# Optimization experiments

Hardware: AMD Instinct MI355X
Metric: run time of the kernel (lower is better)

Reference implementation:

```python
import jax, jax.numpy as jnp
import numpy as np

B, D, E, H, T = 16384, 32, 8, 64, 10  # batch, state_dim, n_experts, hidden, time points
TEMP = 1.0  # gating temperature


def setup_inputs() -> dict:
    key = jax.random.key(0)
    ks = jax.random.split(key, 12)
    w = lambda k, shape, fan_in: (jax.random.normal(k, shape, jnp.float32) / np.sqrt(fan_in)).astype(jnp.float32)
    return {
        "x0": jax.random.normal(ks[0], (B, D), jnp.float32),
        "t_span": jnp.linspace(0.0, 1.0, T).astype(jnp.float32),
        # per-expert time-conditioned MLP: (x, t) -> H -> H -> D
        "W1": w(ks[1], (E, D + 1, H), D + 1), "b1": jnp.zeros((E, H), jnp.float32),
        "W2": w(ks[2], (E, H, H), H),          "b2": jnp.zeros((E, H), jnp.float32),
        "W3": w(ks[3], (E, H, D), H),          "b3": jnp.zeros((E, D), jnp.float32),
        # gating MLP on concat(x, dx_init): 2D -> H -> E
        "Gw1": w(ks[4], (2 * D, H), 2 * D), "Gb1": jnp.zeros((H,), jnp.float32),
        "Gw2": w(ks[5], (H, E), H),         "Gb2": jnp.zeros((E,), jnp.float32),
    }


def _dyn(t, x, W1, b1, W2, b2, W3, b3, Gw1, Gb1, Gw2, Gb2):
    # AME-ODE training-path dynamics: uniform-weighted init, gate, weighted sum
    inp = jnp.concatenate([x, jnp.ones((x.shape[0], 1), x.dtype) * t], axis=-1)  # [B, D+1]
    h = jnp.tanh(jnp.einsum('bi,eih->beh', inp, W1) + b1)
    h = jnp.tanh(jnp.einsum('beh,ehg->beg', h, W2) + b2)
    f = jnp.einsum('beg,egd->bed', h, W3) + b3          # all-expert dynamics [B, E, D]
    dx_init = f.mean(axis=1)                             # uniform weights 1/E
    g = jnp.tanh(jnp.concatenate([x, dx_init], -1) @ Gw1 + Gb1)
    wgt = jax.nn.softmax((g @ Gw2 + Gb2) / TEMP, axis=-1)  # [B, E]
    return jnp.einsum('be,bed->bd', wgt, f)


def reference(x0, t_span, W1, b1, W2, b2, W3, b3, Gw1, Gb1, Gw2, Gb2):
    params = (W1, b1, W2, b2, W3, b3, Gw1, Gb1, Gw2, Gb2)

    def step(x, ts):
        t0, t1 = ts[0], ts[1]
        dt = t1 - t0
        k1 = _dyn(t0, x, *params)
        k2 = _dyn(t0 + 0.5 * dt, x + 0.5 * dt * k1, *params)
        k3 = _dyn(t0 + 0.5 * dt, x + 0.5 * dt * k2, *params)
        k4 = _dyn(t1, x + dt * k3, *params)
        xn = x + (dt / 6.0) * (k1 + 2.0 * k2 + 2.0 * k3 + k4)
        return xn, xn

    pairs = jnp.stack([t_span[:-1], t_span[1:]], axis=1)  # [T-1, 2]
    _, traj = jax.lax.scan(step, x0, pairs)               # [T-1, B, D]
    traj = jnp.concatenate([x0[None], traj], axis=0)       # [T, B, D]
    return jnp.transpose(traj, (1, 0, 2))                  # [B, T, D]
```

## Files before the change

kernel.cpp:

```cpp
#include <hip/hip_runtime.h>
#include <hip/hip_bf16.h>

typedef unsigned int u32;
typedef unsigned short u16;
typedef __attribute__((ext_vector_type(8))) short short8;
typedef __attribute__((ext_vector_type(4))) float f32x4;
typedef __attribute__((ext_vector_type(4))) u32 u32x4;

#define DD 32
#define EE 8
#define HH 64
#define TT 10
#define BATCH 16384
#define EPB 32

__device__ __forceinline__ float fast_tanh(float x) {
  float e = __expf(2.f * x);
  return 1.f - 2.f * __builtin_amdgcn_rcpf(e + 1.f);
}
__device__ __forceinline__ u16 f2b_rn(float v) {
  return (u16)((__float_as_uint(v) + 0x8000u) >> 16);
}
__device__ __forceinline__ u32 pack2_rn(float a, float b) {
  return ((__float_as_uint(a) + 0x8000u) >> 16) |
         ((__float_as_uint(b) + 0x8000u) & 0xffff0000u);
}
__device__ __forceinline__ float unp_lo(u32 p) { return __uint_as_float(p << 16); }
__device__ __forceinline__ float unp_hi(u32 p) { return __uint_as_float(p & 0xffff0000u); }
__device__ __forceinline__ short8 lds_frag(const u32* p) {
  u32x4 w = *(const u32x4*)p;
  return __builtin_bit_cast(short8, w);
}

__global__ __launch_bounds__(512) void ame_ode_kernel(
    const float* __restrict__ x0, const float* __restrict__ tspan,
    const float* __restrict__ W1, const float* __restrict__ b1,
    const float* __restrict__ W2, const float* __restrict__ b2,
    const float* __restrict__ W3, const float* __restrict__ b3,
    const float* __restrict__ Gw1, const float* __restrict__ Gb1,
    const float* __restrict__ Gw2, const float* __restrict__ Gb2,
    float* __restrict__ out)
{
  __shared__ __align__(16) u32 xdb[EPB][36];
  __shared__ __align__(16) u32 fs[EPB][130];
  __shared__ __align__(16) float lg[EPB][9];
  __shared__ __align__(16) u32 hsbuf[EE * 16 * 36];
  __shared__ __align__(16) u16 gw1t[HH][72];
  __shared__ __align__(16) u16 gw2t[16][72];

  const int tid  = threadIdx.x;
  const int lane = tid & 63;
  const int l15  = lane & 15;
  const int quad = lane >> 4;
  const int e    = __builtin_amdgcn_readfirstlane(tid >> 6);
  const int elem = lane & 31;
  const int hf   = lane >> 5;
  const int cc   = 2 * e + hf;
  const int d0   = 2 * cc;
  const int bglob = blockIdx.x * EPB;

  const float* W1f = W1 + e * (DD + 1) * HH;
  const float* b1f = b1 + e * HH;
  const float* W2f = W2 + e * HH * HH;
  const float* b2f = b2 + e * HH;
  const float* W3f = W3 + e * HH * DD;
  const float* b3f = b3 + e * DD;

  short8 bw1[4], bw2[2][4], bw3[2][2];
  #pragma unroll
  for (int nt = 0; nt < 4; nt++)
    #pragma unroll
    for (int j = 0; j < 8; j++)
      bw1[nt][j] = (short)f2b_rn(W1f[(quad * 8 + j) * HH + nt * 16 + l15]);
  #pragma unroll
  for (int ks = 0; ks < 2; ks++)
    #pragma unroll
    for (int nt = 0; nt < 4; nt++)
      #pragma unroll
      for (int j = 0; j < 8; j++)
        bw2[ks][nt][j] = (short)f2b_rn(W2f[(ks * 32 + quad * 8 + j) * HH + nt * 16 + l15]);
  #pragma unroll
  for (int ks = 0; ks < 2; ks++)
    #pragma unroll
    for (int dt2 = 0; dt2 < 2; dt2++)
      #pragma unroll
      for (int j = 0; j < 8; j++)
        bw3[ks][dt2][j] = (short)f2b_rn(W3f[(ks * 32 + quad * 8 + j) * DD + dt2 * 16 + l15]);

  u32 c1p[4], c2p[2], c3p;
  #pragma unroll
  for (int nt = 0; nt < 4; nt++)
    c1p[nt] = pack2_rn(b1f[nt * 16 + l15], W1f[DD * HH + nt * 16 + l15]);
  #pragma unroll
  for (int p = 0; p < 2; p++)
    c2p[p] = pack2_rn(b2f[(2 * p) * 16 + l15], b2f[(2 * p + 1) * 16 + l15]);
  c3p = pack2_rn(b3f[l15], b3f[16 + l15]);
  const float gb1v = Gb1[(e >> 1) * 16 + l15];
  const float gb2v = (l15 < 8) ? Gb2[l15] : 0.f;

  for (int idx = tid; idx < HH * HH; idx += 512) {
    int h = idx >> 6, i = idx & 63;
    gw1t[h][i] = f2b_rn(Gw1[i * HH + h]);
  }
  for (int idx = tid; idx < 16 * HH; idx += 512) {
    int j = idx >> 6, h = idx & 63;
    gw2t[j][h] = (j < EE) ? f2b_rn(Gw2[h * EE + j]) : (u16)0;
  }

  float xst0, xst1, xac0, xac1;
  {
    const float2 v = *(const float2*)(x0 + (bglob + elem) * DD + d0);
    xst0 = v.x; xst1 = v.y; xac0 = v.x; xac1 = v.y;
    xdb[elem][cc] = pack2_rn(v.x, v.y);
    *(float2*)(out + ((bglob + elem) * TT) * DD + d0) = v;
  }
  __syncthreads();

  u32* const hw = hsbuf + e * 576;
  u16* const hw16 = (u16*)hw;
  u16* const fw16 = (u16*)&fs[0][0];
  const u32* const gw1t32 = (const u32*)&gw1t[0][0];
  const u32* const gw2t32 = (const u32*)&gw2t[0][0];
  const u16* const gs16 = (const u16*)hsbuf;
  u16* const gsw16 = (u16*)hsbuf;

  #pragma unroll 1
  for (int step = 0; step < TT - 1; step++) {
    const float t0 = tspan[step];
    const float t1 = tspan[step + 1];
    const float dt = t1 - t0;

    #pragma unroll 1
    for (int s = 0; s < 4; s++) {
      const float tcur = (s == 0) ? t0 : ((s == 3) ? t1 : t0 + 0.5f * dt);

      #pragma unroll
      for (int mt = 0; mt < 2; mt++) {
        const short8 a1 = lds_frag(&xdb[mt * 16 + l15][quad * 4]);
        f32x4 h1a[4];
        #pragma unroll
        for (int nt = 0; nt < 4; nt++) {
          const float iv = __builtin_fmaf(tcur, unp_hi(c1p[nt]), unp_lo(c1p[nt]));
          f32x4 c; c[0] = iv; c[1] = iv; c[2] = iv; c[3] = iv;
          h1a[nt] = __builtin_amdgcn_mfma_f32_16x16x32_bf16(a1, bw1[nt], c, 0, 0, 0);
        }
        #pragma unroll
        for (int nt = 0; nt < 4; nt++)
          #pragma unroll
          for (int r = 0; r < 4; r++)
            hw16[(quad * 4 + r) * 72 + nt * 16 + l15] = f2b_rn(fast_tanh(h1a[nt][r]));

        f32x4 h2a[4];
        #pragma unroll
        for (int nt = 0; nt < 4; nt++) {
          const float bv = (nt & 1) ? unp_hi(c2p[nt >> 1]) : unp_lo(c2p[nt >> 1]);
          f32x4 c; c[0] = bv; c[1] = bv; c[2] = bv; c[3] = bv;
          h2a[nt] = c;
        }
        #pragma unroll
        for (int ks = 0; ks < 2; ks++) {
          const short8 a2 = lds_frag(&hw[l15 * 36 + ks * 16 + quad * 4]);
          #pragma unroll
          for (int nt = 0; nt < 4; nt++)
            h2a[nt] = __builtin_amdgcn_mfma_f32_16x16x32_bf16(a2, bw2[ks][nt], h2a[nt], 0, 0, 0);
        }
        #pragma unroll
        for (int nt = 0; nt < 4; nt++)
          #pragma unroll
          for (int r = 0; r < 4; r++)
            hw16[(quad * 4 + r) * 72 + nt * 16 + l15] = f2b_rn(fast_tanh(h2a[nt][r]));

        f32x4 fa[2];
        #pragma unroll
        for (int dt2 = 0; dt2 < 2; dt2++) {
          const float bv = dt2 ? unp_hi(c3p) : unp_lo(c3p);
          f32x4 c; c[0] = bv; c[1] = bv; c[2] = bv; c[3] = bv;
          fa[dt2] = c;
        }
        #pragma unroll
        for (int ks = 0; ks < 2; ks++) {
          const short8 a3 = lds_frag(&hw[l15 * 36 + ks * 16 + quad * 4]);
          #pragma unroll
          for (int dt2 = 0; dt2 < 2; dt2++)
            fa[dt2] = __builtin_amdgcn_mfma_f32_16x16x32_bf16(a3, bw3[ks][dt2], fa[dt2], 0, 0, 0);
        }
        #pragma unroll
        for (int dt2 = 0; dt2 < 2; dt2++)
          #pragma unroll
          for (int r = 0; r < 4; r++)
            fw16[(mt * 16 + quad * 4 + r) * 260 + e * 32 + dt2 * 16 + l15] = f2b_rn(fa[dt2][r]);
      }
      __syncthreads();

      {
        float s0 = 0.f, s1 = 0.f;
        #pragma unroll
        for (int j = 0; j < EE; j++) {
          const u32 p = fs[elem][j * 16 + cc];
          s0 += unp_lo(p); s1 += unp_hi(p);
        }
        xdb[elem][16 + cc] = pack2_rn(s0 * 0.125f, s1 * 0.125f);
      }
      __syncthreads();

      {
        const int mt = e & 1, nt = e >> 1;
        f32x4 u; u[0] = gb1v; u[1] = gb1v; u[2] = gb1v; u[3] = gb1v;
        #pragma unroll
        for (int ks = 0; ks < 2; ks++) {
          const short8 ag = lds_frag(&xdb[mt * 16 + l15][ks * 16 + quad * 4]);
          const short8 bg = lds_frag(&gw1t32[(nt * 16 + l15) * 36 + ks * 16 + quad * 4]);
          u = __builtin_amdgcn_mfma_f32_16x16x32_bf16(ag, bg, u, 0, 0, 0);
        }
        #pragma unroll
        for (int r = 0; r < 4; r++)
          gsw16[(mt * 16 + quad * 4 + r) * 72 + nt * 16 + l15] = f2b_rn(fast_tanh(u[r]));
      }
      __syncthreads();

      if (e < 2) {
        const int mt = e;
        f32x4 lv; lv[0] = gb2v; lv[1] = gb2v; lv[2] = gb2v; lv[3] = gb2v;
        #pragma unroll
        for (int ks = 0; ks < 2; ks++) {
          const short8 ag = lds_frag((const u32*)&gs16[(mt * 16 + l15) * 72 + ks * 32 + quad * 8]);
          const short8 bg = lds_frag(&gw2t32[l15 * 36 + ks * 16 + quad * 4]);
          lv = __builtin_amdgcn_mfma_f32_16x16x32_bf16(ag, bg, lv, 0, 0, 0);
        }
        if (l15 < 8) {
          #pragma unroll
          for (int r = 0; r < 4; r++)
            lg[mt * 16 + quad * 4 + r][l15] = lv[r];
        }
      }
      __syncthreads();

      {
        float la[EE];
        #pragma unroll
        for (int j = 0; j < EE; j++) la[j] = lg[elem][j];
        float m = la[0];
        #pragma unroll
        for (int j = 1; j < EE; j++) m = fmaxf(m, la[j]);
        float w8[EE], ss = 0.f;
        #pragma unroll
        for (int j = 0; j < EE; j++) { w8[j] = __expf(la[j] - m); ss += w8[j]; }
        const float inv = __builtin_amdgcn_rcpf(ss);

        float k0 = 0.f, k1 = 0.f;
        #pragma unroll
        for (int j = 0; j < EE; j++) {
          const float wg = w8[j] * inv;
          const u32 p = fs[elem][j * 16 + cc];
          k0 = __builtin_fmaf(wg, unp_lo(p), k0);
          k1 = __builtin_fmaf(wg, unp_hi(p), k1);
        }

        const float wk = (s == 1 || s == 2) ? 2.f : 1.f;
        const float ak = dt * (1.f / 6.f) * wk;
        xac0 = __builtin_fmaf(ak, k0, xac0);
        xac1 = __builtin_fmaf(ak, k1, xac1);

        float xn0, xn1;
        if (s < 3) {
          const float cn = (s == 2) ? dt : 0.5f * dt;
          xn0 = __builtin_fmaf(cn, k0, xst0);
          xn1 = __builtin_fmaf(cn, k1, xst1);
        } else {
          xst0 = xac0; xst1 = xac1; xn0 = xac0; xn1 = xac1;
          float2 o; o.x = xn0; o.y = xn1;
          *(float2*)(out + ((bglob + elem) * TT + step + 1) * DD + d0) = o;
        }
        xdb[elem][cc] = pack2_rn(xn0, xn1);
      }
      __syncthreads();
    }
  }
}

extern "C" void kernel_launch(void* const* d_in, const int* in_sizes, int n_in,
                              void* d_out, int out_size, void* d_ws, size_t ws_size,
                              hipStream_t stream)
{
  const float* x0    = (const float*)d_in[0];
  const float* tspan = (const float*)d_in[1];
  const float* W1  = (const float*)d_in[2];
  const float* b1  = (const float*)d_in[3];
  const float* W2  = (const float*)d_in[4];
  const float* b2  = (const float*)d_in[5];
  const float* W3  = (const float*)d_in[6];
  const float* b3  = (const float*)d_in[7];
  const float* Gw1 = (const float*)d_in[8];
  const float* Gb1 = (const float*)d_in[9];
  const float* Gw2 = (const float*)d_in[10];
  const float* Gb2 = (const float*)d_in[11];

  ame_ode_kernel<<<BATCH / EPB, 512, 0, stream>>>(
      x0, tspan, W1, b1, W2, b2, W3, b3, Gw1, Gb1, Gw2, Gb2, (float*)d_out);
}
```

Baseline: 370.4 us.

## Double batch tile per block and keep gating weights in registers

Raises the number of batch elements per 512-thread block from 32 to 64, so each wave handles four M-tiles and all 64 lanes own one element with four state dims. The gating MLP weights move out of transposed LDS copies into per-wave register fragments, and both gating layers are spread over more waves. Biases are pre-broadcast once per stage and bf16 packing uses a single perm instruction. This amortises barriers and per-stage setup over more work, but halves the grid to 256 blocks and raises register and LDS pressure.

```diff
diff --git a/kernel.cpp b/kernel.cpp
--- a/kernel.cpp
+++ b/kernel.cpp
@@ -6,13 +6,14 @@
 typedef __attribute__((ext_vector_type(8))) short short8;
 typedef __attribute__((ext_vector_type(4))) float f32x4;
 typedef __attribute__((ext_vector_type(4))) u32 u32x4;
+typedef __attribute__((ext_vector_type(2))) u32 u32x2;
 
 #define DD 32
 #define EE 8
 #define HH 64
 #define TT 10
 #define BATCH 16384
-#define EPB 32
+#define EPB 64
 
 __device__ __forceinline__ float fast_tanh(float x) {
   float e = __expf(2.f * x);
@@ -22,8 +23,8 @@
   return (u16)((__float_as_uint(v) + 0x8000u) >> 16);
 }
 __device__ __forceinline__ u32 pack2_rn(float a, float b) {
-  return ((__float_as_uint(a) + 0x8000u) >> 16) |
-         ((__float_as_uint(b) + 0x8000u) & 0xffff0000u);
+  return __builtin_amdgcn_perm(__float_as_uint(b) + 0x8000u,
+                               __float_as_uint(a) + 0x8000u, 0x07060302u);
 }
 __device__ __forceinline__ float unp_lo(u32 p) { return __uint_as_float(p << 16); }
 __device__ __forceinline__ float unp_hi(u32 p) { return __uint_as_float(p & 0xffff0000u); }
@@ -31,6 +32,7 @@
   u32x4 w = *(const u32x4*)p;
   return __builtin_bit_cast(short8, w);
 }
+__device__ __forceinline__ f32x4 bcast4(float v) { f32x4 c; c[0]=v; c[1]=v; c[2]=v; c[3]=v; return c; }
 
 __global__ __launch_bounds__(512) void ame_ode_kernel(
     const float* __restrict__ x0, const float* __restrict__ tspan,
@@ -43,21 +45,15 @@
 {
   __shared__ __align__(16) u32 xdb[EPB][36];
   __shared__ __align__(16) u32 fs[EPB][130];
-  __shared__ __align__(16) float lg[EPB][9];
+  __shared__ __align__(16) float lg[EPB][12];
   __shared__ __align__(16) u32 hsbuf[EE * 16 * 36];
-  __shared__ __align__(16) u16 gw1t[HH][72];
-  __shared__ __align__(16) u16 gw2t[16][72];
 
   const int tid  = threadIdx.x;
   const int lane = tid & 63;
   const int l15  = lane & 15;
   const int quad = lane >> 4;
   const int e    = __builtin_amdgcn_readfirstlane(tid >> 6);
-  const int elem = lane & 31;
-  const int hf   = lane >> 5;
-  const int cc   = 2 * e + hf;
-  const int d0   = 2 * cc;
-  const int bglob = blockIdx.x * EPB;
+  const int b    = blockIdx.x * EPB + lane;
 
   const float* W1f = W1 + e * (DD + 1) * HH;
   const float* b1f = b1 + e * HH;
@@ -87,42 +83,56 @@
       for (int j = 0; j < 8; j++)
         bw3[ks][dt2][j] = (short)f2b_rn(W3f[(ks * 32 + quad * 8 + j) * DD + dt2 * 16 + l15]);
 
-  u32 c1p[4], c2p[2], c3p;
+  const int g1mt = e & 3;
+  const int g1n0 = (e >> 2) * 2;
+  short8 bg1[2][2];
+  #pragma unroll
+  for (int ni = 0; ni < 2; ni++)
+    #pragma unroll
+    for (int ks = 0; ks < 2; ks++)
+      #pragma unroll
+      for (int j = 0; j < 8; j++)
+        bg1[ni][ks][j] = (short)f2b_rn(Gw1[(ks * 32 + quad * 8 + j) * HH + (g1n0 + ni) * 16 + l15]);
+  const float gb1a = Gb1[g1n0 * 16 + l15];
+  const float gb1b = Gb1[(g1n0 + 1) * 16 + l15];
+
+  short8 bg2[2];
+  float gb2v = 0.f;
+  if (e < 4) {
+    #pragma unroll
+    for (int ks = 0; ks < 2; ks++)
+      #pragma unroll
+      for (int j = 0; j < 8; j++)
+        bg2[ks][j] = (short)((l15 < 8) ? f2b_rn(Gw2[(ks * 32 + quad * 8 + j) * EE + l15]) : 0);
+    gb2v = (l15 < 8) ? Gb2[l15] : 0.f;
+  }
+
+  u32 c1p[4];
   #pragma unroll
   for (int nt = 0; nt < 4; nt++)
     c1p[nt] = pack2_rn(b1f[nt * 16 + l15], W1f[DD * HH + nt * 16 + l15]);
-  #pragma unroll
-  for (int p = 0; p < 2; p++)
-    c2p[p] = pack2_rn(b2f[(2 * p) * 16 + l15], b2f[(2 * p + 1) * 16 + l15]);
-  c3p = pack2_rn(b3f[l15], b3f[16 + l15]);
-  const float gb1v = Gb1[(e >> 1) * 16 + l15];
-  const float gb2v = (l15 < 8) ? Gb2[l15] : 0.f;
-
-  for (int idx = tid; idx < HH * HH; idx += 512) {
-    int h = idx >> 6, i = idx & 63;
-    gw1t[h][i] = f2b_rn(Gw1[i * HH + h]);
-  }
-  for (int idx = tid; idx < 16 * HH; idx += 512) {
-    int j = idx >> 6, h = idx & 63;
-    gw2t[j][h] = (j < EE) ? f2b_rn(Gw2[h * EE + j]) : (u16)0;
-  }
-
-  float xst0, xst1, xac0, xac1;
+  f32x4 c2i[4], c3i[2];
+  #pragma unroll
+  for (int nt = 0; nt < 4; nt++) c2i[nt] = bcast4(b2f[nt * 16 + l15]);
+  #pragma unroll
+  for (int dt2 = 0; dt2 < 2; dt2++) c3i[dt2] = bcast4(b3f[dt2 * 16 + l15]);
+
+  float xst[4], xacc[4];
   {
-    const float2 v = *(const float2*)(x0 + (bglob + elem) * DD + d0);
-    xst0 = v.x; xst1 = v.y; xac0 = v.x; xac1 = v.y;
-    xdb[elem][cc] = pack2_rn(v.x, v.y);
-    *(float2*)(out + ((bglob + elem) * TT) * DD + d0) = v;
+    const float4 v = *(const float4*)(x0 + b * DD + 4 * e);
+    xst[0] = v.x; xst[1] = v.y; xst[2] = v.z; xst[3] = v.w;
+    xacc[0] = v.x; xacc[1] = v.y; xacc[2] = v.z; xacc[3] = v.w;
+    u32x2 p; p.x = pack2_rn(v.x, v.y); p.y = pack2_rn(v.z, v.w);
+    *(u32x2*)&xdb[lane][2 * e] = p;
+    *(float4*)(out + b * TT * DD + 4 * e) = v;
   }
   __syncthreads();
 
-  u32* const hw = hsbuf + e * 576;
+  u32* const hw   = hsbuf + e * 576;
   u16* const hw16 = (u16*)hw;
   u16* const fw16 = (u16*)&fs[0][0];
-  const u32* const gw1t32 = (const u32*)&gw1t[0][0];
-  const u32* const gw2t32 = (const u32*)&gw2t[0][0];
-  const u16* const gs16 = (const u16*)hsbuf;
-  u16* const gsw16 = (u16*)hsbuf;
+  u16* const uw16 = (u16*)hsbuf;
+  const u32* const u32v = hsbuf;
 
   #pragma unroll 1
   for (int step = 0; step < TT - 1; step++) {
@@ -134,16 +144,18 @@
     for (int s = 0; s < 4; s++) {
       const float tcur = (s == 0) ? t0 : ((s == 3) ? t1 : t0 + 0.5f * dt);
 
-      #pragma unroll
-      for (int mt = 0; mt < 2; mt++) {
+      f32x4 c1i[4];
+      #pragma unroll
+      for (int nt = 0; nt < 4; nt++)
+        c1i[nt] = bcast4(__builtin_fmaf(tcur, unp_hi(c1p[nt]), unp_lo(c1p[nt])));
+
+      #pragma unroll 2
+      for (int mt = 0; mt < 4; mt++) {
         const short8 a1 = lds_frag(&xdb[mt * 16 + l15][quad * 4]);
         f32x4 h1a[4];
         #pragma unroll
-        for (int nt = 0; nt < 4; nt++) {
-          const float iv = __builtin_fmaf(tcur, unp_hi(c1p[nt]), unp_lo(c1p[nt]));
-          f32x4 c; c[0] = iv; c[1] = iv; c[2] = iv; c[3] = iv;
-          h1a[nt] = __builtin_amdgcn_mfma_f32_16x16x32_bf16(a1, bw1[nt], c, 0, 0, 0);
-        }
+        for (int nt = 0; nt < 4; nt++)
+          h1a[nt] = __builtin_amdgcn_mfma_f32_16x16x32_bf16(a1, bw1[nt], c1i[nt], 0, 0, 0);
         #pragma unroll
         for (int nt = 0; nt < 4; nt++)
           #pragma unroll
@@ -152,11 +164,7 @@
 
         f32x4 h2a[4];
         #pragma unroll
-        for (int nt = 0; nt < 4; nt++) {
-          const float bv = (nt & 1) ? unp_hi(c2p[nt >> 1]) : unp_lo(c2p[nt >> 1]);
-          f32x4 c; c[0] = bv; c[1] = bv; c[2] = bv; c[3] = bv;
-          h2a[nt] = c;
-        }
+        for (int nt = 0; nt < 4; nt++) h2a[nt] = c2i[nt];
         #pragma unroll
         for (int ks = 0; ks < 2; ks++) {
           const short8 a2 = lds_frag(&hw[l15 * 36 + ks * 16 + quad * 4]);
@@ -172,11 +180,7 @@
 
         f32x4 fa[2];
         #pragma unroll
-        for (int dt2 = 0; dt2 < 2; dt2++) {
-          const float bv = dt2 ? unp_hi(c3p) : unp_lo(c3p);
-          f32x4 c; c[0] = bv; c[1] = bv; c[2] = bv; c[3] = bv;
-          fa[dt2] = c;
-        }
+        for (int dt2 = 0; dt2 < 2; dt2++) fa[dt2] = c3i[dt2];
         #pragma unroll
         for (int ks = 0; ks < 2; ks++) {
           const short8 a3 = lds_frag(&hw[l15 * 36 + ks * 16 + quad * 4]);
@@ -193,85 +197,94 @@
       __syncthreads();
 
       {
-        float s0 = 0.f, s1 = 0.f;
+        float s0 = 0.f, s1 = 0.f, s2 = 0.f, s3 = 0.f;
         #pragma unroll
         for (int j = 0; j < EE; j++) {
-          const u32 p = fs[elem][j * 16 + cc];
-          s0 += unp_lo(p); s1 += unp_hi(p);
-        }
-        xdb[elem][16 + cc] = pack2_rn(s0 * 0.125f, s1 * 0.125f);
+          const u32x2 p = *(const u32x2*)&fs[lane][j * 16 + 2 * e];
+          s0 += unp_lo(p.x); s1 += unp_hi(p.x);
+          s2 += unp_lo(p.y); s3 += unp_hi(p.y);
+        }
+        u32x2 w; w.x = pack2_rn(s0 * 0.125f, s1 * 0.125f);
+        w.y = pack2_rn(s2 * 0.125f, s3 * 0.125f);
+        *(u32x2*)&xdb[lane][16 + 2 * e] = w;
       }
       __syncthreads();
 
       {
-        const int mt = e & 1, nt = e >> 1;
-        f32x4 u; u[0] = gb1v; u[1] = gb1v; u[2] = gb1v; u[3] = gb1v;
+        f32x4 u0 = bcast4(gb1a), u1 = bcast4(gb1b);
         #pragma unroll
         for (int ks = 0; ks < 2; ks++) {
-          const short8 ag = lds_frag(&xdb[mt * 16 + l15][ks * 16 + quad * 4]);
-          const short8 bg = lds_frag(&gw1t32[(nt * 16 + l15) * 36 + ks * 16 + quad * 4]);
-          u = __builtin_amdgcn_mfma_f32_16x16x32_bf16(ag, bg, u, 0, 0, 0);
-        }
-        #pragma unroll
-        for (int r = 0; r < 4; r++)
-          gsw16[(mt * 16 + quad * 4 + r) * 72 + nt * 16 + l15] = f2b_rn(fast_tanh(u[r]));
-      }
-      __syncthreads();
-
-      if (e < 2) {
-        const int mt = e;
-        f32x4 lv; lv[0] = gb2v; lv[1] = gb2v; lv[2] = gb2v; lv[3] = gb2v;
+          const short8 ag = lds_frag(&xdb[g1mt * 16 + l15][ks * 16 + quad * 4]);
+          u0 = __builtin_amdgcn_mfma_f32_16x16x32_bf16(ag, bg1[0][ks], u0, 0, 0, 0);
+          u1 = __builtin_amdgcn_mfma_f32_16x16x32_bf16(ag, bg1[1][ks], u1, 0, 0, 0);
+        }
+        #pragma unroll
+        for (int r = 0; r < 4; r++) {
+          uw16[(g1mt * 16 + quad * 4 + r) * 72 + g1n0 * 16 + l15]       = f2b_rn(fast_tanh(u0[r]));
+          uw16[(g1mt * 16 + quad * 4 + r) * 72 + (g1n0 + 1) * 16 + l15] = f2b_rn(fast_tanh(u1[r]));
+        }
+      }
+      __syncthreads();
+
+      if (e < 4) {
+        f32x4 lv = bcast4(gb2v);
         #pragma unroll
         for (int ks = 0; ks < 2; ks++) {
-          const short8 ag = lds_frag((const u32*)&gs16[(mt * 16 + l15) * 72 + ks * 32 + quad * 8]);
-          const short8 bg = lds_frag(&gw2t32[l15 * 36 + ks * 16 + quad * 4]);
-          lv = __builtin_amdgcn_mfma_f32_16x16x32_bf16(ag, bg, lv, 0, 0, 0);
+          const short8 ag = lds_frag(&u32v[(e * 16 + l15) * 36 + ks * 16 + quad * 4]);
+          lv = __builtin_amdgcn_mfma_f32_16x16x32_bf16(ag, bg2[ks], lv, 0, 0, 0);
         }
         if (l15 < 8) {
           #pragma unroll
           for (int r = 0; r < 4; r++)
-            lg[mt * 16 + quad * 4 + r][l15] = lv[r];
+            lg[e * 16 + quad * 4 + r][l15] = lv[r];
         }
       }
       __syncthreads();
 
       {
-        float la[EE];
-        #pragma unroll
-        for (int j = 0; j < EE; j++) la[j] = lg[elem][j];
-        float m = la[0];
-        #pragma unroll
-        for (int j = 1; j < EE; j++) m = fmaxf(m, la[j]);
-        float w8[EE], ss = 0.f;
-        #pragma unroll
-        for (int j = 0; j < EE; j++) { w8[j] = __expf(la[j] - m); ss += w8[j]; }
+        const float4 la0 = *(const float4*)&lg[lane][0];
+        const float4 la1 = *(const float4*)&lg[lane][4];
+        float m = fmaxf(fmaxf(fmaxf(la0.x, la0.y), fmaxf(la0.z, la0.w)),
+                        fmaxf(fmaxf(la1.x, la1.y), fmaxf(la1.z, la1.w)));
+        float w8[EE];
+        w8[0] = __expf(la0.x - m); w8[1] = __expf(la0.y - m);
+        w8[2] = __expf(la0.z - m); w8[3] = __expf(la0.w - m);
+        w8[4] = __expf(la1.x - m); w8[5] = __expf(la1.y - m);
+        w8[6] = __expf(la1.z - m); w8[7] = __expf(la1.w - m);
+        float ss = 0.f;
+        #pragma unroll
+        for (int j = 0; j < EE; j++) ss += w8[j];
         const float inv = __builtin_amdgcn_rcpf(ss);
 
-        float k0 = 0.f, k1 = 0.f;
+        float kc[4] = {0.f, 0.f, 0.f, 0.f};
         #pragma unroll
         for (int j = 0; j < EE; j++) {
           const float wg = w8[j] * inv;
-          const u32 p = fs[elem][j * 16 + cc];
-          k0 = __builtin_fmaf(wg, unp_lo(p), k0);
-          k1 = __builtin_fmaf(wg, unp_hi(p), k1);
+          const u32x2 p = *(const u32x2*)&fs[lane][j * 16 + 2 * e];
+          kc[0] = __builtin_fmaf(wg, unp_lo(p.x), kc[0]);
+          kc[1] = __builtin_fmaf(wg, unp_hi(p.x), kc[1]);
+          kc[2] = __builtin_fmaf(wg, unp_lo(p.y), kc[2]);
+          kc[3] = __builtin_fmaf(wg, unp_hi(p.y), kc[3]);
         }
 
         const float wk = (s == 1 || s == 2) ? 2.f : 1.f;
         const float ak = dt * (1.f / 6.f) * wk;
-        xac0 = __builtin_fmaf(ak, k0, xac0);
-        xac1 = __builtin_fmaf(ak, k1, xac1);
-
-        float xn0, xn1;
+        #pragma unroll
+        for (int q = 0; q < 4; q++) xacc[q] = __builtin_fmaf(ak, kc[q], xacc[q]);
+
+        float xn[4];
         if (s < 3) {
           const float cn = (s == 2) ? dt : 0.5f * dt;
-          xn0 = __builtin_fmaf(cn, k0, xst0);
-          xn1 = __builtin_fmaf(cn, k1, xst1);
+          #pragma unroll
+          for (int q = 0; q < 4; q++) xn[q] = __builtin_fmaf(cn, kc[q], xst[q]);
         } else {
-          xst0 = xac0; xst1 = xac1; xn0 = xac0; xn1 = xac1;
-          float2 o; o.x = xn0; o.y = xn1;
-          *(float2*)(out + ((bglob + elem) * TT + step + 1) * DD + d0) = o;
-        }
-        xdb[elem][cc] = pack2_rn(xn0, xn1);
+          #pragma unroll
+          for (int q = 0; q < 4; q++) { xst[q] = xacc[q]; xn[q] = xacc[q]; }
+          float4 o; o.x = xn[0]; o.y = xn[1]; o.z = xn[2]; o.w = xn[3];
+          *(float4*)(out + (b * TT + step + 1) * DD + 4 * e) = o;
+        }
+        u32x2 p; p.x = pack2_rn(xn[0], xn[1]); p.y = pack2_rn(xn[2], xn[3]);
+        *(u32x2*)&xdb[lane][2 * e] = p;
       }
       __syncthreads();
     }
```

Result: faster. 328.9 us (-11.2%).
